# Performance work log

Measured on AMD Instinct MI355X. Metric: run time of the kernel, lower is better.

Reference implementation:

```python
import jax, jax.numpy as jnp
import numpy as np

L, D, H, DR, KF = 2, 256, 8, 64, 4   # n_layer, d_model, n_head, d_rpe, k_feedforward
B, S, T = 2, 256, 256
LN_EPS = 1e-5


def _ln(x, g, b):
    m = jnp.mean(x, -1, keepdims=True)
    v = jnp.mean((x - m) ** 2, -1, keepdims=True)
    return (x - m) * jax.lax.rsqrt(v + LN_EPS) * g + b


def _attn_rpe(q_in, kv_in, rpe, tgt_mask, wq, bq, wk, bk, wv, bv, wo, bo, wr, br):
    # RPE-biased multi-head cross attention: rpe -> (rpe_k, rpe_v) added per (src,tgt) pair.
    Bq, Sq, _ = q_in.shape
    Tk = kv_in.shape[1]
    Dh = D // H
    q = (q_in @ wq + bq).reshape(Bq, Sq, H, Dh)
    k = (kv_in @ wk + bk).reshape(Bq, Tk, H, Dh)
    v = (kv_in @ wv + bv).reshape(Bq, Tk, H, Dh)
    r = rpe @ wr + br                                   # [B,S,T,2D]
    rk, rv = jnp.split(r, 2, axis=-1)
    rk = rk.reshape(Bq, Sq, Tk, H, Dh)
    rv = rv.reshape(Bq, Sq, Tk, H, Dh)
    scale = 1.0 / np.sqrt(Dh).astype(np.float32)
    scores = (jnp.einsum('bshd,bthd->bhst', q, k)
              + jnp.einsum('bshd,bsthd->bhst', q, rk)) * scale
    scores = jnp.where(tgt_mask[:, None, None, :], -jnp.inf, scores)
    w = jax.nn.softmax(scores, axis=-1)                 # [B,H,S,T]
    out = (jnp.einsum('bhst,bthd->bshd', w, v)
           + jnp.einsum('bhst,bsthd->bshd', w, rv))
    return out.reshape(Bq, Sq, D) @ wo + bo


def _forward(src, tgt, rpe, src_padding_mask, tgt_padding_mask, p):
    for i in range(L):  # loop over n_layer (structurally distinct params)
        s2 = _ln(src, p['ln1_g'][i], p['ln1_b'][i])
        tn = _ln(tgt, p['lnt_g'][i], p['lnt_b'][i])
        a = _attn_rpe(s2, tn, rpe, tgt_padding_mask,
                      p['wq'][i], p['bq'][i], p['wk'][i], p['bk'][i],
                      p['wv'][i], p['bv'][i], p['wo'][i], p['bo'][i],
                      p['wr'][i], p['br'][i])
        src = src + a
        s2 = _ln(src, p['ln2_g'][i], p['ln2_b'][i])
        s2 = jax.nn.relu(s2 @ p['w1'][i] + p['b1'][i]) @ p['w2'][i] + p['b2'][i]
        src = src + s2
        src = jnp.where(src_padding_mask[:, :, None], 0.0, src)
    return src


def setup_inputs() -> dict:
    key = jax.random.key(0)
    ks = jax.random.split(key, 16)
    f = lambda k, shp: (0.02 * jax.random.normal(k, shp)).astype(jnp.float32)
    return {
        'src': jax.random.normal(ks[0], (B, S, D), jnp.float32),
        'tgt': jax.random.normal(ks[1], (B, T, D), jnp.float32),
        'rpe': jax.random.normal(ks[2], (B, S, T, DR), jnp.float32),
        'src_padding_mask': jax.random.bernoulli(ks[3], 0.05, (B, S)),
        'tgt_padding_mask': jax.random.bernoulli(ks[4], 0.1, (B, T)),
        'ln1_g': jnp.ones((L, D), jnp.float32), 'ln1_b': jnp.zeros((L, D), jnp.float32),
        'lnt_g': jnp.ones((L, D), jnp.float32), 'lnt_b': jnp.zeros((L, D), jnp.float32),
        'ln2_g': jnp.ones((L, D), jnp.float32), 'ln2_b': jnp.zeros((L, D), jnp.float32),
        'wq': f(ks[5], (L, D, D)), 'bq': jnp.zeros((L, D), jnp.float32),
        'wk': f(ks[6], (L, D, D)), 'bk': jnp.zeros((L, D), jnp.float32),
        'wv': f(ks[7], (L, D, D)), 'bv': jnp.zeros((L, D), jnp.float32),
        'wo': f(ks[8], (L, D, D)), 'bo': jnp.zeros((L, D), jnp.float32),
        'wr': f(ks[9], (L, DR, 2 * D)), 'br': jnp.zeros((L, 2 * D), jnp.float32),
        'w1': f(ks[10], (L, D, KF * D)), 'b1': jnp.zeros((L, KF * D), jnp.float32),
        'w2': f(ks[11], (L, KF * D, D)), 'b2': jnp.zeros((L, D), jnp.float32),
    }


def reference(src, tgt, rpe, src_padding_mask, tgt_padding_mask,
              ln1_g, ln1_b, lnt_g, lnt_b, ln2_g, ln2_b,
              wq, bq, wk, bk, wv, bv, wo, bo, wr, br, w1, b1, w2, b2):
    p = dict(ln1_g=ln1_g, ln1_b=ln1_b, lnt_g=lnt_g, lnt_b=lnt_b,
             ln2_g=ln2_g, ln2_b=ln2_b, wq=wq, bq=bq, wk=wk, bk=bk,
             wv=wv, bv=bv, wo=wo, bo=bo, wr=wr, br=br,
             w1=w1, b1=b1, w2=w2, b2=b2)
    return _forward(src, tgt, rpe, src_padding_mask, tgt_padding_mask, p)
```

## Files before the change

kernel.cpp:

```cpp
#include <hip/hip_runtime.h>
#include <math.h>

#define ROWS 512
#define DMODEL 256
#define NH 8
#define DH 32
#define NEG_INF -1e30f

__global__ __launch_bounds__(64) void ln_qt_kernel(
    const float* __restrict__ src, const float* __restrict__ tgt,
    const float* __restrict__ g1, const float* __restrict__ b1,
    const float* __restrict__ gt, const float* __restrict__ bt,
    const float* __restrict__ bo,
    float* __restrict__ S2, float* __restrict__ TNb, float* __restrict__ X)
{
  int row = blockIdx.x;
  const float* x; float* o; const float* g; const float* b;
  if (row < ROWS) { x = src + row * DMODEL; o = S2 + row * DMODEL; g = g1; b = b1; }
  else { int r = row - ROWS; x = tgt + r * DMODEL; o = TNb + r * DMODEL; g = gt; b = bt; }
  int lane = threadIdx.x;
  float4 v = ((const float4*)x)[lane];
  float s  = v.x + v.y + v.z + v.w;
  float ss = v.x*v.x + v.y*v.y + v.z*v.z + v.w*v.w;
#pragma unroll
  for (int off = 32; off >= 1; off >>= 1) {
    s  += __shfl_xor(s,  off);
    ss += __shfl_xor(ss, off);
  }
  float mean = s * (1.0f / 256.0f);
  float var  = ss * (1.0f / 256.0f) - mean * mean;
  float rstd = rsqrtf(var + 1e-5f);
  float4 gg = ((const float4*)g)[lane];
  float4 bb = ((const float4*)b)[lane];
  float4 ov;
  ov.x = (v.x - mean) * rstd * gg.x + bb.x;
  ov.y = (v.y - mean) * rstd * gg.y + bb.y;
  ov.z = (v.z - mean) * rstd * gg.z + bb.z;
  ov.w = (v.w - mean) * rstd * gg.w + bb.w;
  ((float4*)o)[lane] = ov;
  if (row < ROWS) {
    float4 bov = ((const float4*)bo)[lane];
    float4 xi;
    xi.x = v.x + bov.x; xi.y = v.y + bov.y; xi.z = v.z + bov.z; xi.w = v.w + bov.w;
    ((float4*)(X + row * DMODEL))[lane] = xi;
  }
}

__global__ __launch_bounds__(64) void ln2_kernel(
    const float* __restrict__ X, const float* __restrict__ g, const float* __restrict__ b,
    const float* __restrict__ b2, const int* __restrict__ smask,
    float* __restrict__ XN, float* __restrict__ outinit)
{
  int row = blockIdx.x;
  int lane = threadIdx.x;
  float4 v = ((const float4*)(X + row * DMODEL))[lane];
  float s  = v.x + v.y + v.z + v.w;
  float ss = v.x*v.x + v.y*v.y + v.z*v.z + v.w*v.w;
#pragma unroll
  for (int off = 32; off >= 1; off >>= 1) {
    s  += __shfl_xor(s,  off);
    ss += __shfl_xor(ss, off);
  }
  float mean = s * (1.0f / 256.0f);
  float var  = ss * (1.0f / 256.0f) - mean * mean;
  float rstd = rsqrtf(var + 1e-5f);
  float4 gg = ((const float4*)g)[lane];
  float4 bb = ((const float4*)b)[lane];
  float4 ov;
  ov.x = (v.x - mean) * rstd * gg.x + bb.x;
  ov.y = (v.y - mean) * rstd * gg.y + bb.y;
  ov.z = (v.z - mean) * rstd * gg.z + bb.z;
  ov.w = (v.w - mean) * rstd * gg.w + bb.w;
  ((float4*)(XN + row * DMODEL))[lane] = ov;
  float mm = (smask[row] != 0) ? 0.0f : 1.0f;
  float4 b2v = ((const float4*)b2)[lane];
  float4 oi;
  oi.x = mm * (v.x + b2v.x);
  oi.y = mm * (v.y + b2v.y);
  oi.z = mm * (v.z + b2v.z);
  oi.w = mm * (v.w + b2v.w);
  ((float4*)(outinit + row * DMODEL))[lane] = oi;
}

__device__ __forceinline__ void gemm_core32(
    const float* __restrict__ A, int lda,
    const float* __restrict__ Bw, int ldb,
    int kbeg, int kend, int m0, int n0,
    float acc[2][4])
{
  __shared__ float At[32][34];
  __shared__ float Bs[32][64];
  int tid = threadIdx.x;
  int tx = tid & 15, ty = tid >> 4;
  int r  = tid >> 3;
  int c4 = tid & 7;
  for (int kc = kbeg; kc < kend; kc += 32) {
    float4 a = *(const float4*)(A + (size_t)(m0 + r) * lda + kc + c4 * 4);
    const float* bp = Bw + (size_t)(kc + r) * ldb + n0;
    float4 b0 = *(const float4*)(bp + c4 * 4);
    float4 b1v = *(const float4*)(bp + 32 + c4 * 4);
    At[c4*4+0][r] = a.x; At[c4*4+1][r] = a.y; At[c4*4+2][r] = a.z; At[c4*4+3][r] = a.w;
    *(float4*)&Bs[r][c4*4]      = b0;
    *(float4*)&Bs[r][32 + c4*4] = b1v;
    __syncthreads();
#pragma unroll
    for (int k = 0; k < 32; ++k) {
      float2 av = *(const float2*)&At[k][ty * 2];
      float4 bv = *(const float4*)&Bs[k][tx * 4];
      acc[0][0] = fmaf(av.x, bv.x, acc[0][0]); acc[0][1] = fmaf(av.x, bv.y, acc[0][1]);
      acc[0][2] = fmaf(av.x, bv.z, acc[0][2]); acc[0][3] = fmaf(av.x, bv.w, acc[0][3]);
      acc[1][0] = fmaf(av.y, bv.x, acc[1][0]); acc[1][1] = fmaf(av.y, bv.y, acc[1][1]);
      acc[1][2] = fmaf(av.y, bv.z, acc[1][2]); acc[1][3] = fmaf(av.y, bv.w, acc[1][3]);
    }
    __syncthreads();
  }
}

__global__ __launch_bounds__(256) void qkv_kernel(
    const float* __restrict__ S2, const float* __restrict__ TNb,
    const float* __restrict__ wq, const float* __restrict__ wk, const float* __restrict__ wv,
    const float* __restrict__ bq, const float* __restrict__ bk, const float* __restrict__ bv,
    float* __restrict__ Qb, float* __restrict__ Kb, float* __restrict__ Vb)
{
  int z = blockIdx.z;
  const float* A    = (z == 0) ? S2 : TNb;
  const float* Bw   = (z == 0) ? wq : (z == 1) ? wk : wv;
  const float* bias = (z == 0) ? bq : (z == 1) ? bk : bv;
  int m0 = blockIdx.y * 32, n0 = blockIdx.x * 64;
  float acc[2][4] = {};
  gemm_core32(A, DMODEL, Bw, DMODEL, 0, DMODEL, m0, n0, acc);
  int tid = threadIdx.x, tx = tid & 15, ty = tid >> 4;
  int c0 = n0 + tx * 4;
  const float scale = 0.1767766952966369f;
#pragma unroll
  for (int i = 0; i < 2; ++i) {
    int m = m0 + ty * 2 + i;
    float4 r;
    r.x = acc[i][0] + bias[c0 + 0];
    r.y = acc[i][1] + bias[c0 + 1];
    r.z = acc[i][2] + bias[c0 + 2];
    r.w = acc[i][3] + bias[c0 + 3];
    if (z == 0) {
      r.x *= scale; r.y *= scale; r.z *= scale; r.w *= scale;
      *(float4*)&Qb[m * DMODEL + c0] = r;
    } else {
      int b = m >> 8, t = m & 255, h = c0 >> 5, d0 = c0 & 31;
      float* dst = ((z == 1) ? Kb : Vb) + (size_t)(b * NH + h) * 8192 + t * DH + d0;
      *(float4*)dst = r;
    }
  }
}

__global__ __launch_bounds__(256) void wo_kernel(
    const float* __restrict__ AO, const float* __restrict__ wo,
    float* __restrict__ X)
{
  int m0 = blockIdx.y * 32, n0 = blockIdx.x * 64;
  int kbeg = blockIdx.z * 128;
  float acc[2][4] = {};
  gemm_core32(AO, DMODEL, wo, DMODEL, kbeg, kbeg + 128, m0, n0, acc);
  int tid = threadIdx.x, tx = tid & 15, ty = tid >> 4;
  int c0 = n0 + tx * 4;
#pragma unroll
  for (int i = 0; i < 2; ++i) {
    int m = m0 + ty * 2 + i;
    atomicAdd(&X[m * DMODEL + c0 + 0], acc[i][0]);
    atomicAdd(&X[m * DMODEL + c0 + 1], acc[i][1]);
    atomicAdd(&X[m * DMODEL + c0 + 2], acc[i][2]);
    atomicAdd(&X[m * DMODEL + c0 + 3], acc[i][3]);
  }
}

__global__ __launch_bounds__(256) void ff1_kernel(
    const float* __restrict__ XN, const float* __restrict__ w1, const float* __restrict__ b1,
    float* __restrict__ H1)
{
  int m0 = blockIdx.y * 32, n0 = blockIdx.x * 64;
  float acc[2][4] = {};
  gemm_core32(XN, DMODEL, w1, 1024, 0, DMODEL, m0, n0, acc);
  int tid = threadIdx.x, tx = tid & 15, ty = tid >> 4;
  int c0 = n0 + tx * 4;
#pragma unroll
  for (int i = 0; i < 2; ++i) {
    int m = m0 + ty * 2 + i;
    float4 r;
    r.x = fmaxf(acc[i][0] + b1[c0 + 0], 0.0f);
    r.y = fmaxf(acc[i][1] + b1[c0 + 1], 0.0f);
    r.z = fmaxf(acc[i][2] + b1[c0 + 2], 0.0f);
    r.w = fmaxf(acc[i][3] + b1[c0 + 3], 0.0f);
    *(float4*)&H1[m * 1024 + c0] = r;
  }
}

__global__ __launch_bounds__(256) void ff2_kernel(
    const float* __restrict__ H1, const float* __restrict__ w2,
    const int* __restrict__ smask, float* __restrict__ outb)
{
  int m0 = blockIdx.y * 32, n0 = blockIdx.x * 64;
  int kbeg = blockIdx.z * 256;
  float acc[2][4] = {};
  gemm_core32(H1, 1024, w2, DMODEL, kbeg, kbeg + 256, m0, n0, acc);
  int tid = threadIdx.x, tx = tid & 15, ty = tid >> 4;
  int c0 = n0 + tx * 4;
#pragma unroll
  for (int i = 0; i < 2; ++i) {
    int m = m0 + ty * 2 + i;
    float mm = (smask[m] != 0) ? 0.0f : 1.0f;
    atomicAdd(&outb[m * DMODEL + c0 + 0], mm * acc[i][0]);
    atomicAdd(&outb[m * DMODEL + c0 + 1], mm * acc[i][1]);
    atomicAdd(&outb[m * DMODEL + c0 + 2], mm * acc[i][2]);
    atomicAdd(&outb[m * DMODEL + c0 + 3], mm * acc[i][3]);
  }
}

__global__ __launch_bounds__(256) void attn_kernel(
    const float* __restrict__ Qb, const float* __restrict__ Kb, const float* __restrict__ Vb,
    const float* __restrict__ rpe, const int* __restrict__ tmask,
    const float* __restrict__ wrl, const float* __restrict__ brl,
    float* __restrict__ AO)
{
  __shared__ float Ks[256][32];
  __shared__ float Vt[32][260];
  __shared__ float ps[4][256];
  __shared__ float qs[16][32];
  __shared__ float wks[5][32];
  __shared__ float wvs[5][32];
  int bid = blockIdx.x;
  int b = bid >> 7, h = (bid >> 4) & 7, s0 = (bid & 15) << 4;
  int tid = threadIdx.x;
  const float* Kp = Kb + (size_t)(b * NH + h) * 8192;
  const float* Vp = Vb + (size_t)(b * NH + h) * 8192;
  {
    int t = tid;
    const float4* kr = (const float4*)(Kp + t * DH);
    const float4* vr = (const float4*)(Vp + t * DH);
    int sw = t & 7;
#pragma unroll
    for (int c = 0; c < 8; ++c) {
      float4 k4 = kr[c];
      *(float4*)&Ks[t][(c ^ sw) * 4] = k4;
    }
#pragma unroll
    for (int c = 0; c < 8; ++c) {
      float4 v4 = vr[c];
      Vt[c*4+0][t] = v4.x; Vt[c*4+1][t] = v4.y; Vt[c*4+2][t] = v4.z; Vt[c*4+3][t] = v4.w;
    }
  }
  if (tid < 160) {
    int j = tid >> 5, d = tid & 31;
    wks[j][d] = (j < 4) ? wrl[j * 512 + h * DH + d]       : brl[h * DH + d];
    wvs[j][d] = (j < 4) ? wrl[j * 512 + 256 + h * DH + d] : brl[256 + h * DH + d];
  }
  if (tid >= 128) {
    int u = tid - 128;
    int rr = u >> 3, cc = u & 7;
    *(float4*)&qs[rr][cc*4] =
        *(const float4*)&Qb[(b * 256 + s0 + rr) * DMODEL + h * DH + cc * 4];
  }
  __syncthreads();

  int w = tid >> 6, lane = tid & 63;
  int msk[4];
#pragma unroll
  for (int it = 0; it < 4; ++it) msk[it] = tmask[b * 256 + it * 64 + lane];

  for (int i = 0; i < 4; ++i) {
    int sl = w * 4 + i;
    int s = s0 + sl;
    float4 q4[8];
#pragma unroll
    for (int c = 0; c < 8; ++c) q4[c] = *(const float4*)&qs[sl][c * 4];
    float qw[4]; float qbr = 0.0f;
#pragma unroll
    for (int j = 0; j < 4; ++j) {
      float t0 = 0;
#pragma unroll
      for (int c = 0; c < 8; ++c) {
        float4 wv4 = *(const float4*)&wks[j][c * 4];
        t0 += q4[c].x*wv4.x + q4[c].y*wv4.y + q4[c].z*wv4.z + q4[c].w*wv4.w;
      }
      qw[j] = t0;
    }
#pragma unroll
    for (int c = 0; c < 8; ++c) {
      float4 wv4 = *(const float4*)&wks[4][c * 4];
      qbr += q4[c].x*wv4.x + q4[c].y*wv4.y + q4[c].z*wv4.z + q4[c].w*wv4.w;
    }
    const float4* rp4 = (const float4*)(rpe + (size_t)(b * 256 + s) * 1024);
    float sc[4]; float4 rr[4];
#pragma unroll
    for (int it = 0; it < 4; ++it) {
      int t = it * 64 + lane;
      int sw = t & 7;
      float sv = 0;
#pragma unroll
      for (int c = 0; c < 8; ++c) {
        float4 k4 = *(const float4*)&Ks[t][(c ^ sw) * 4];
        sv = fmaf(q4[c].x, k4.x, sv); sv = fmaf(q4[c].y, k4.y, sv);
        sv = fmaf(q4[c].z, k4.z, sv); sv = fmaf(q4[c].w, k4.w, sv);
      }
      float4 rv = rp4[t];
      rr[it] = rv;
      sv += rv.x*qw[0] + rv.y*qw[1] + rv.z*qw[2] + rv.w*qw[3] + qbr;
      if (msk[it] != 0) sv = NEG_INF;
      sc[it] = sv;
    }
    float mval = fmaxf(fmaxf(sc[0], sc[1]), fmaxf(sc[2], sc[3]));
#pragma unroll
    for (int off = 32; off >= 1; off >>= 1) mval = fmaxf(mval, __shfl_xor(mval, off));
    float p[4], lsum = 0;
#pragma unroll
    for (int it = 0; it < 4; ++it) { p[it] = __expf(sc[it] - mval); lsum += p[it]; }
    float wj0 = 0, wj1 = 0, wj2 = 0, wj3 = 0;
#pragma unroll
    for (int it = 0; it < 4; ++it) {
      wj0 = fmaf(p[it], rr[it].x, wj0);
      wj1 = fmaf(p[it], rr[it].y, wj1);
      wj2 = fmaf(p[it], rr[it].z, wj2);
      wj3 = fmaf(p[it], rr[it].w, wj3);
    }
#pragma unroll
    for (int off = 32; off >= 1; off >>= 1) {
      lsum += __shfl_xor(lsum, off);
      wj0 += __shfl_xor(wj0, off);
      wj1 += __shfl_xor(wj1, off);
      wj2 += __shfl_xor(wj2, off);
      wj3 += __shfl_xor(wj3, off);
    }
#pragma unroll
    for (int it = 0; it < 4; ++it) ps[w][it * 64 + lane] = p[it];
    int g = lane >> 5, d = lane & 31;
    float o = 0;
#pragma unroll
    for (int n = 0; n < 32; ++n) {
      int t = g * 128 + n * 4;
      float4 p4 = *(const float4*)&ps[w][t];
      float4 v4 = *(const float4*)&Vt[d][t];
      o += p4.x*v4.x + p4.y*v4.y + p4.z*v4.z + p4.w*v4.w;
    }
    o += __shfl_xor(o, 32);
    float corr = wj0 * wvs[0][d] + wj1 * wvs[1][d] + wj2 * wvs[2][d] + wj3 * wvs[3][d];
    float oval = (o + corr) / lsum + wvs[4][d];
    if (lane < 32) AO[(b * 256 + s) * DMODEL + h * DH + d] = oval;
  }
}

extern "C" void kernel_launch(void* const* d_in, const int* in_sizes, int n_in,
                              void* d_out, int out_size, void* d_ws, size_t ws_size,
                              hipStream_t stream)
{
  const float* src  = (const float*)d_in[0];
  const float* tgt  = (const float*)d_in[1];
  const float* rpe  = (const float*)d_in[2];
  const int*   smask = (const int*)d_in[3];
  const int*   tmask = (const int*)d_in[4];
  const float* ln1g = (const float*)d_in[5];
  const float* ln1b = (const float*)d_in[6];
  const float* lntg = (const float*)d_in[7];
  const float* lntb = (const float*)d_in[8];
  const float* ln2g = (const float*)d_in[9];
  const float* ln2b = (const float*)d_in[10];
  const float* wq = (const float*)d_in[11];
  const float* bq = (const float*)d_in[12];
  const float* wk = (const float*)d_in[13];
  const float* bk = (const float*)d_in[14];
  const float* wv = (const float*)d_in[15];
  const float* bv = (const float*)d_in[16];
  const float* wo = (const float*)d_in[17];
  const float* bo = (const float*)d_in[18];
  const float* wr = (const float*)d_in[19];
  const float* br = (const float*)d_in[20];
  const float* w1 = (const float*)d_in[21];
  const float* b1 = (const float*)d_in[22];
  const float* w2 = (const float*)d_in[23];
  const float* b2 = (const float*)d_in[24];

  float* w    = (float*)d_ws;
  float* S2   = w;
  float* TNb  = w + 131072;
  float* Qb   = w + 262144;
  float* Kb   = w + 393216;
  float* Vb   = w + 524288;
  float* AO   = w + 655360;
  float* X    = w + 786432;
  float* XN   = w + 917504;
  float* SRC1 = w + 1048576;
  float* H1   = w + 1179648;

  for (int l = 0; l < 2; ++l) {
    const float* srcin = l ? SRC1 : src;
    float* outb = l ? (float*)d_out : SRC1;
    ln_qt_kernel<<<1024, 64, 0, stream>>>(srcin, tgt, ln1g + l*256, ln1b + l*256,
                                          lntg + l*256, lntb + l*256, bo + l*256,
                                          S2, TNb, X);
    qkv_kernel<<<dim3(4, 16, 3), 256, 0, stream>>>(S2, TNb,
                                                   wq + l*65536, wk + l*65536, wv + l*65536,
                                                   bq + l*256, bk + l*256, bv + l*256,
                                                   Qb, Kb, Vb);
    attn_kernel<<<256, 256, 0, stream>>>(Qb, Kb, Vb, rpe, tmask,
                                         wr + l*2048, br + l*512, AO);
    wo_kernel<<<dim3(4, 16, 2), 256, 0, stream>>>(AO, wo + l*65536, X);
    ln2_kernel<<<512, 64, 0, stream>>>(X, ln2g + l*256, ln2b + l*256, b2 + l*256,
                                       smask, XN, outb);
    ff1_kernel<<<dim3(16, 16), 256, 0, stream>>>(XN, w1 + l*262144, b1 + l*1024, H1);
    ff2_kernel<<<dim3(4, 16, 4), 256, 0, stream>>>(H1, w2 + l*262144, smask, outb);
  }
}
```

Before: 262.8 us.

## Fuse all layer stages into one persistent kernel with grid barriers

Replaces the fourteen per-stage kernel launches with a single persistent 256-block kernel. Stages are separated by software grid-wide barriers built on an atomic counter, and shared memory is a union of the attention and GEMM layouts. The aim is to remove launch overhead and inter-kernel gaps. In exchange it relies on all 256 blocks being co-resident to avoid deadlock, adds barrier spin cost, and changes the split-K factor of the wo GEMM.

```diff
diff --git a/kernel.cpp b/kernel.cpp
--- a/kernel.cpp
+++ b/kernel.cpp
@@ -1,103 +1,53 @@
 #include <hip/hip_runtime.h>
 #include <math.h>
 
-#define ROWS 512
-#define DMODEL 256
-#define NH 8
-#define DH 32
 #define NEG_INF -1e30f
 
-__global__ __launch_bounds__(64) void ln_qt_kernel(
-    const float* __restrict__ src, const float* __restrict__ tgt,
-    const float* __restrict__ g1, const float* __restrict__ b1,
-    const float* __restrict__ gt, const float* __restrict__ bt,
-    const float* __restrict__ bo,
-    float* __restrict__ S2, float* __restrict__ TNb, float* __restrict__ X)
-{
-  int row = blockIdx.x;
-  const float* x; float* o; const float* g; const float* b;
-  if (row < ROWS) { x = src + row * DMODEL; o = S2 + row * DMODEL; g = g1; b = b1; }
-  else { int r = row - ROWS; x = tgt + r * DMODEL; o = TNb + r * DMODEL; g = gt; b = bt; }
-  int lane = threadIdx.x;
-  float4 v = ((const float4*)x)[lane];
-  float s  = v.x + v.y + v.z + v.w;
-  float ss = v.x*v.x + v.y*v.y + v.z*v.z + v.w*v.w;
-#pragma unroll
-  for (int off = 32; off >= 1; off >>= 1) {
-    s  += __shfl_xor(s,  off);
-    ss += __shfl_xor(ss, off);
+struct AttnLds {
+  float Ks[256][32];
+  float Vt[32][260];
+  float ps[4][256];
+  float qs[16][32];
+  float wks[5][32];
+  float wvs[5][32];
+};
+struct GemmLds {
+  float At[32][34];
+  float Bs[32][64];
+};
+union MegaLds {
+  AttnLds a;
+  GemmLds g;
+  float pad[20608];
+};
+
+__device__ __forceinline__ void gbar(unsigned* cnt, unsigned expect) {
+  __syncthreads();
+  if (threadIdx.x == 0) {
+    __threadfence();
+    __hip_atomic_fetch_add(cnt, 1u, __ATOMIC_RELEASE, __HIP_MEMORY_SCOPE_AGENT);
+    while (__hip_atomic_load(cnt, __ATOMIC_RELAXED, __HIP_MEMORY_SCOPE_AGENT) < expect)
+      __builtin_amdgcn_s_sleep(2);
+    __threadfence();
   }
-  float mean = s * (1.0f / 256.0f);
-  float var  = ss * (1.0f / 256.0f) - mean * mean;
-  float rstd = rsqrtf(var + 1e-5f);
-  float4 gg = ((const float4*)g)[lane];
-  float4 bb = ((const float4*)b)[lane];
-  float4 ov;
-  ov.x = (v.x - mean) * rstd * gg.x + bb.x;
-  ov.y = (v.y - mean) * rstd * gg.y + bb.y;
-  ov.z = (v.z - mean) * rstd * gg.z + bb.z;
-  ov.w = (v.w - mean) * rstd * gg.w + bb.w;
-  ((float4*)o)[lane] = ov;
-  if (row < ROWS) {
-    float4 bov = ((const float4*)bo)[lane];
-    float4 xi;
-    xi.x = v.x + bov.x; xi.y = v.y + bov.y; xi.z = v.z + bov.z; xi.w = v.w + bov.w;
-    ((float4*)(X + row * DMODEL))[lane] = xi;
-  }
+  __syncthreads();
 }
 
-__global__ __launch_bounds__(64) void ln2_kernel(
-    const float* __restrict__ X, const float* __restrict__ g, const float* __restrict__ b,
-    const float* __restrict__ b2, const int* __restrict__ smask,
-    float* __restrict__ XN, float* __restrict__ outinit)
-{
-  int row = blockIdx.x;
-  int lane = threadIdx.x;
-  float4 v = ((const float4*)(X + row * DMODEL))[lane];
-  float s  = v.x + v.y + v.z + v.w;
-  float ss = v.x*v.x + v.y*v.y + v.z*v.z + v.w*v.w;
-#pragma unroll
-  for (int off = 32; off >= 1; off >>= 1) {
-    s  += __shfl_xor(s,  off);
-    ss += __shfl_xor(ss, off);
-  }
-  float mean = s * (1.0f / 256.0f);
-  float var  = ss * (1.0f / 256.0f) - mean * mean;
-  float rstd = rsqrtf(var + 1e-5f);
-  float4 gg = ((const float4*)g)[lane];
-  float4 bb = ((const float4*)b)[lane];
-  float4 ov;
-  ov.x = (v.x - mean) * rstd * gg.x + bb.x;
-  ov.y = (v.y - mean) * rstd * gg.y + bb.y;
-  ov.z = (v.z - mean) * rstd * gg.z + bb.z;
-  ov.w = (v.w - mean) * rstd * gg.w + bb.w;
-  ((float4*)(XN + row * DMODEL))[lane] = ov;
-  float mm = (smask[row] != 0) ? 0.0f : 1.0f;
-  float4 b2v = ((const float4*)b2)[lane];
-  float4 oi;
-  oi.x = mm * (v.x + b2v.x);
-  oi.y = mm * (v.y + b2v.y);
-  oi.z = mm * (v.z + b2v.z);
-  oi.w = mm * (v.w + b2v.w);
-  ((float4*)(outinit + row * DMODEL))[lane] = oi;
-}
-
-__device__ __forceinline__ void gemm_core32(
+__device__ __forceinline__ void gemm32(MegaLds& L,
     const float* __restrict__ A, int lda,
     const float* __restrict__ Bw, int ldb,
-    int kbeg, int kend, int m0, int n0,
-    float acc[2][4])
+    int kbeg, int kend, int m0, int n0, float acc[2][4])
 {
-  __shared__ float At[32][34];
-  __shared__ float Bs[32][64];
+  float (&At)[32][34] = L.g.At;
+  float (&Bs)[32][64] = L.g.Bs;
   int tid = threadIdx.x;
-  int tx = tid & 15, ty = tid >> 4;
   int r  = tid >> 3;
   int c4 = tid & 7;
+  int tx = tid & 15, ty = tid >> 4;
   for (int kc = kbeg; kc < kend; kc += 32) {
     float4 a = *(const float4*)(A + (size_t)(m0 + r) * lda + kc + c4 * 4);
     const float* bp = Bw + (size_t)(kc + r) * ldb + n0;
-    float4 b0 = *(const float4*)(bp + c4 * 4);
+    float4 b0  = *(const float4*)(bp + c4 * 4);
     float4 b1v = *(const float4*)(bp + 32 + c4 * 4);
     At[c4*4+0][r] = a.x; At[c4*4+1][r] = a.y; At[c4*4+2][r] = a.z; At[c4*4+3][r] = a.w;
     *(float4*)&Bs[r][c4*4]      = b0;
@@ -116,232 +66,327 @@
   }
 }
 
-__global__ __launch_bounds__(256) void qkv_kernel(
-    const float* __restrict__ S2, const float* __restrict__ TNb,
-    const float* __restrict__ wq, const float* __restrict__ wk, const float* __restrict__ wv,
-    const float* __restrict__ bq, const float* __restrict__ bk, const float* __restrict__ bv,
-    float* __restrict__ Qb, float* __restrict__ Kb, float* __restrict__ Vb)
+__global__ __launch_bounds__(256, 1) void mega_kernel(
+    const float* __restrict__ src, const float* __restrict__ tgt,
+    const float* __restrict__ rpe,
+    const int* __restrict__ smask, const int* __restrict__ tmask,
+    const float* __restrict__ ln1g, const float* __restrict__ ln1b,
+    const float* __restrict__ lntg, const float* __restrict__ lntb,
+    const float* __restrict__ ln2g, const float* __restrict__ ln2b,
+    const float* __restrict__ wq, const float* __restrict__ bq,
+    const float* __restrict__ wk, const float* __restrict__ bk,
+    const float* __restrict__ wv, const float* __restrict__ bv,
+    const float* __restrict__ wo, const float* __restrict__ bo,
+    const float* __restrict__ wr, const float* __restrict__ br,
+    const float* __restrict__ w1, const float* __restrict__ b1,
+    const float* __restrict__ w2, const float* __restrict__ b2,
+    float* __restrict__ ws, float* __restrict__ out, unsigned* __restrict__ cnt)
 {
-  int z = blockIdx.z;
-  const float* A    = (z == 0) ? S2 : TNb;
-  const float* Bw   = (z == 0) ? wq : (z == 1) ? wk : wv;
-  const float* bias = (z == 0) ? bq : (z == 1) ? bk : bv;
-  int m0 = blockIdx.y * 32, n0 = blockIdx.x * 64;
-  float acc[2][4] = {};
-  gemm_core32(A, DMODEL, Bw, DMODEL, 0, DMODEL, m0, n0, acc);
-  int tid = threadIdx.x, tx = tid & 15, ty = tid >> 4;
-  int c0 = n0 + tx * 4;
-  const float scale = 0.1767766952966369f;
-#pragma unroll
-  for (int i = 0; i < 2; ++i) {
-    int m = m0 + ty * 2 + i;
-    float4 r;
-    r.x = acc[i][0] + bias[c0 + 0];
-    r.y = acc[i][1] + bias[c0 + 1];
-    r.z = acc[i][2] + bias[c0 + 2];
-    r.w = acc[i][3] + bias[c0 + 3];
-    if (z == 0) {
-      r.x *= scale; r.y *= scale; r.z *= scale; r.w *= scale;
-      *(float4*)&Qb[m * DMODEL + c0] = r;
-    } else {
-      int b = m >> 8, t = m & 255, h = c0 >> 5, d0 = c0 & 31;
-      float* dst = ((z == 1) ? Kb : Vb) + (size_t)(b * NH + h) * 8192 + t * DH + d0;
-      *(float4*)dst = r;
-    }
-  }
-}
-
-__global__ __launch_bounds__(256) void wo_kernel(
-    const float* __restrict__ AO, const float* __restrict__ wo,
-    float* __restrict__ X)
-{
-  int m0 = blockIdx.y * 32, n0 = blockIdx.x * 64;
-  int kbeg = blockIdx.z * 128;
-  float acc[2][4] = {};
-  gemm_core32(AO, DMODEL, wo, DMODEL, kbeg, kbeg + 128, m0, n0, acc);
-  int tid = threadIdx.x, tx = tid & 15, ty = tid >> 4;
-  int c0 = n0 + tx * 4;
-#pragma unroll
-  for (int i = 0; i < 2; ++i) {
-    int m = m0 + ty * 2 + i;
-    atomicAdd(&X[m * DMODEL + c0 + 0], acc[i][0]);
-    atomicAdd(&X[m * DMODEL + c0 + 1], acc[i][1]);
-    atomicAdd(&X[m * DMODEL + c0 + 2], acc[i][2]);
-    atomicAdd(&X[m * DMODEL + c0 + 3], acc[i][3]);
-  }
-}
-
-__global__ __launch_bounds__(256) void ff1_kernel(
-    const float* __restrict__ XN, const float* __restrict__ w1, const float* __restrict__ b1,
-    float* __restrict__ H1)
-{
-  int m0 = blockIdx.y * 32, n0 = blockIdx.x * 64;
-  float acc[2][4] = {};
-  gemm_core32(XN, DMODEL, w1, 1024, 0, DMODEL, m0, n0, acc);
-  int tid = threadIdx.x, tx = tid & 15, ty = tid >> 4;
-  int c0 = n0 + tx * 4;
-#pragma unroll
-  for (int i = 0; i < 2; ++i) {
-    int m = m0 + ty * 2 + i;
-    float4 r;
-    r.x = fmaxf(acc[i][0] + b1[c0 + 0], 0.0f);
-    r.y = fmaxf(acc[i][1] + b1[c0 + 1], 0.0f);
-    r.z = fmaxf(acc[i][2] + b1[c0 + 2], 0.0f);
-    r.w = fmaxf(acc[i][3] + b1[c0 + 3], 0.0f);
-    *(float4*)&H1[m * 1024 + c0] = r;
-  }
-}
-
-__global__ __launch_bounds__(256) void ff2_kernel(
-    const float* __restrict__ H1, const float* __restrict__ w2,
-    const int* __restrict__ smask, float* __restrict__ outb)
-{
-  int m0 = blockIdx.y * 32, n0 = blockIdx.x * 64;
-  int kbeg = blockIdx.z * 256;
-  float acc[2][4] = {};
-  gemm_core32(H1, 1024, w2, DMODEL, kbeg, kbeg + 256, m0, n0, acc);
-  int tid = threadIdx.x, tx = tid & 15, ty = tid >> 4;
-  int c0 = n0 + tx * 4;
-#pragma unroll
-  for (int i = 0; i < 2; ++i) {
-    int m = m0 + ty * 2 + i;
-    float mm = (smask[m] != 0) ? 0.0f : 1.0f;
-    atomicAdd(&outb[m * DMODEL + c0 + 0], mm * acc[i][0]);
-    atomicAdd(&outb[m * DMODEL + c0 + 1], mm * acc[i][1]);
-    atomicAdd(&outb[m * DMODEL + c0 + 2], mm * acc[i][2]);
-    atomicAdd(&outb[m * DMODEL + c0 + 3], mm * acc[i][3]);
-  }
-}
-
-__global__ __launch_bounds__(256) void attn_kernel(
-    const float* __restrict__ Qb, const float* __restrict__ Kb, const float* __restrict__ Vb,
-    const float* __restrict__ rpe, const int* __restrict__ tmask,
-    const float* __restrict__ wrl, const float* __restrict__ brl,
-    float* __restrict__ AO)
-{
-  __shared__ float Ks[256][32];
-  __shared__ float Vt[32][260];
-  __shared__ float ps[4][256];
-  __shared__ float qs[16][32];
-  __shared__ float wks[5][32];
-  __shared__ float wvs[5][32];
-  int bid = blockIdx.x;
-  int b = bid >> 7, h = (bid >> 4) & 7, s0 = (bid & 15) << 4;
-  int tid = threadIdx.x;
-  const float* Kp = Kb + (size_t)(b * NH + h) * 8192;
-  const float* Vp = Vb + (size_t)(b * NH + h) * 8192;
-  {
-    int t = tid;
-    const float4* kr = (const float4*)(Kp + t * DH);
-    const float4* vr = (const float4*)(Vp + t * DH);
-    int sw = t & 7;
-#pragma unroll
-    for (int c = 0; c < 8; ++c) {
-      float4 k4 = kr[c];
-      *(float4*)&Ks[t][(c ^ sw) * 4] = k4;
-    }
-#pragma unroll
-    for (int c = 0; c < 8; ++c) {
-      float4 v4 = vr[c];
-      Vt[c*4+0][t] = v4.x; Vt[c*4+1][t] = v4.y; Vt[c*4+2][t] = v4.z; Vt[c*4+3][t] = v4.w;
-    }
-  }
-  if (tid < 160) {
-    int j = tid >> 5, d = tid & 31;
-    wks[j][d] = (j < 4) ? wrl[j * 512 + h * DH + d]       : brl[h * DH + d];
-    wvs[j][d] = (j < 4) ? wrl[j * 512 + 256 + h * DH + d] : brl[256 + h * DH + d];
-  }
-  if (tid >= 128) {
-    int u = tid - 128;
-    int rr = u >> 3, cc = u & 7;
-    *(float4*)&qs[rr][cc*4] =
-        *(const float4*)&Qb[(b * 256 + s0 + rr) * DMODEL + h * DH + cc * 4];
-  }
-  __syncthreads();
-
+  __shared__ MegaLds L;
+  int tid = threadIdx.x, bx = blockIdx.x;
   int w = tid >> 6, lane = tid & 63;
-  int msk[4];
-#pragma unroll
-  for (int it = 0; it < 4; ++it) msk[it] = tmask[b * 256 + it * 64 + lane];
-
-  for (int i = 0; i < 4; ++i) {
-    int sl = w * 4 + i;
-    int s = s0 + sl;
-    float4 q4[8];
-#pragma unroll
-    for (int c = 0; c < 8; ++c) q4[c] = *(const float4*)&qs[sl][c * 4];
-    float qw[4]; float qbr = 0.0f;
-#pragma unroll
-    for (int j = 0; j < 4; ++j) {
-      float t0 = 0;
-#pragma unroll
-      for (int c = 0; c < 8; ++c) {
-        float4 wv4 = *(const float4*)&wks[j][c * 4];
-        t0 += q4[c].x*wv4.x + q4[c].y*wv4.y + q4[c].z*wv4.z + q4[c].w*wv4.w;
-      }
-      qw[j] = t0;
-    }
-#pragma unroll
-    for (int c = 0; c < 8; ++c) {
-      float4 wv4 = *(const float4*)&wks[4][c * 4];
-      qbr += q4[c].x*wv4.x + q4[c].y*wv4.y + q4[c].z*wv4.z + q4[c].w*wv4.w;
-    }
-    const float4* rp4 = (const float4*)(rpe + (size_t)(b * 256 + s) * 1024);
-    float sc[4]; float4 rr[4];
-#pragma unroll
-    for (int it = 0; it < 4; ++it) {
-      int t = it * 64 + lane;
-      int sw = t & 7;
-      float sv = 0;
-#pragma unroll
-      for (int c = 0; c < 8; ++c) {
-        float4 k4 = *(const float4*)&Ks[t][(c ^ sw) * 4];
-        sv = fmaf(q4[c].x, k4.x, sv); sv = fmaf(q4[c].y, k4.y, sv);
-        sv = fmaf(q4[c].z, k4.z, sv); sv = fmaf(q4[c].w, k4.w, sv);
-      }
-      float4 rv = rp4[t];
-      rr[it] = rv;
-      sv += rv.x*qw[0] + rv.y*qw[1] + rv.z*qw[2] + rv.w*qw[3] + qbr;
-      if (msk[it] != 0) sv = NEG_INF;
-      sc[it] = sv;
-    }
-    float mval = fmaxf(fmaxf(sc[0], sc[1]), fmaxf(sc[2], sc[3]));
-#pragma unroll
-    for (int off = 32; off >= 1; off >>= 1) mval = fmaxf(mval, __shfl_xor(mval, off));
-    float p[4], lsum = 0;
-#pragma unroll
-    for (int it = 0; it < 4; ++it) { p[it] = __expf(sc[it] - mval); lsum += p[it]; }
-    float wj0 = 0, wj1 = 0, wj2 = 0, wj3 = 0;
-#pragma unroll
-    for (int it = 0; it < 4; ++it) {
-      wj0 = fmaf(p[it], rr[it].x, wj0);
-      wj1 = fmaf(p[it], rr[it].y, wj1);
-      wj2 = fmaf(p[it], rr[it].z, wj2);
-      wj3 = fmaf(p[it], rr[it].w, wj3);
-    }
-#pragma unroll
-    for (int off = 32; off >= 1; off >>= 1) {
-      lsum += __shfl_xor(lsum, off);
-      wj0 += __shfl_xor(wj0, off);
-      wj1 += __shfl_xor(wj1, off);
-      wj2 += __shfl_xor(wj2, off);
-      wj3 += __shfl_xor(wj3, off);
-    }
-#pragma unroll
-    for (int it = 0; it < 4; ++it) ps[w][it * 64 + lane] = p[it];
-    int g = lane >> 5, d = lane & 31;
-    float o = 0;
-#pragma unroll
-    for (int n = 0; n < 32; ++n) {
-      int t = g * 128 + n * 4;
-      float4 p4 = *(const float4*)&ps[w][t];
-      float4 v4 = *(const float4*)&Vt[d][t];
-      o += p4.x*v4.x + p4.y*v4.y + p4.z*v4.z + p4.w*v4.w;
-    }
-    o += __shfl_xor(o, 32);
-    float corr = wj0 * wvs[0][d] + wj1 * wvs[1][d] + wj2 * wvs[2][d] + wj3 * wvs[3][d];
-    float oval = (o + corr) / lsum + wvs[4][d];
-    if (lane < 32) AO[(b * 256 + s) * DMODEL + h * DH + d] = oval;
+  unsigned bi = 0;
+
+  float* S2   = ws;
+  float* TN   = ws + 131072;
+  float* Qb   = ws + 262144;
+  float* Kb   = ws + 393216;
+  float* Vb   = ws + 524288;
+  float* AO   = ws + 655360;
+  float* X    = ws + 786432;
+  float* XN   = ws + 917504;
+  float* SRC1 = ws + 1048576;
+  float* H1   = ws + 1179648;
+
+  for (int l = 0; l < 2; ++l) {
+    const float* srcin = l ? SRC1 : src;
+    float* outb = l ? out : SRC1;
+    const float* g1 = ln1g + l*256; const float* be1 = ln1b + l*256;
+    const float* gt = lntg + l*256; const float* bet = lntb + l*256;
+    const float* g2 = ln2g + l*256; const float* be2 = ln2b + l*256;
+    const float* wq_l = wq + l*65536; const float* bq_l = bq + l*256;
+    const float* wk_l = wk + l*65536; const float* bk_l = bk + l*256;
+    const float* wv_l = wv + l*65536; const float* bv_l = bv + l*256;
+    const float* wo_l = wo + l*65536; const float* bo_l = bo + l*256;
+    const float* wr_l = wr + l*2048;  const float* br_l = br + l*512;
+    const float* w1_l = w1 + l*262144; const float* b1_l = b1 + l*1024;
+    const float* w2_l = w2 + l*262144; const float* b2_l = b2 + l*256;
+
+    {
+      int task = bx * 4 + w;
+      bool issrc = task < 512;
+      int r = issrc ? task : task - 512;
+      const float* xrow = issrc ? srcin + r * 256 : tgt + r * 256;
+      float* orow       = issrc ? S2 + r * 256    : TN + r * 256;
+      const float* g    = issrc ? g1 : gt;
+      const float* bb   = issrc ? be1 : bet;
+      float4 v = ((const float4*)xrow)[lane];
+      float s  = v.x + v.y + v.z + v.w;
+      float ss = v.x*v.x + v.y*v.y + v.z*v.z + v.w*v.w;
+#pragma unroll
+      for (int off = 32; off >= 1; off >>= 1) {
+        s  += __shfl_xor(s,  off);
+        ss += __shfl_xor(ss, off);
+      }
+      float mean = s * (1.0f / 256.0f);
+      float var  = ss * (1.0f / 256.0f) - mean * mean;
+      float rstd = rsqrtf(var + 1e-5f);
+      float4 gg = ((const float4*)g)[lane];
+      float4 b4 = ((const float4*)bb)[lane];
+      float4 ov;
+      ov.x = (v.x - mean) * rstd * gg.x + b4.x;
+      ov.y = (v.y - mean) * rstd * gg.y + b4.y;
+      ov.z = (v.z - mean) * rstd * gg.z + b4.z;
+      ov.w = (v.w - mean) * rstd * gg.w + b4.w;
+      ((float4*)orow)[lane] = ov;
+      if (issrc) {
+        float4 bov = ((const float4*)bo_l)[lane];
+        float4 xi;
+        xi.x = v.x + bov.x; xi.y = v.y + bov.y; xi.z = v.z + bov.z; xi.w = v.w + bov.w;
+        ((float4*)(X + r * 256))[lane] = xi;
+      }
+    }
+    gbar(cnt, ++bi * 256u);
+
+    if (bx < 192) {
+      int z = bx >> 6, u = bx & 63;
+      int m0 = (u >> 2) * 32, n0 = (u & 3) * 64;
+      const float* A    = (z == 0) ? S2 : TN;
+      const float* Bw   = (z == 0) ? wq_l : (z == 1) ? wk_l : wv_l;
+      const float* bias = (z == 0) ? bq_l : (z == 1) ? bk_l : bv_l;
+      float acc[2][4] = {};
+      gemm32(L, A, 256, Bw, 256, 0, 256, m0, n0, acc);
+      int tx = tid & 15, ty = tid >> 4;
+      int c0 = n0 + tx * 4;
+      const float scale = 0.1767766952966369f;
+#pragma unroll
+      for (int i = 0; i < 2; ++i) {
+        int m = m0 + ty * 2 + i;
+        float4 r;
+        r.x = acc[i][0] + bias[c0 + 0];
+        r.y = acc[i][1] + bias[c0 + 1];
+        r.z = acc[i][2] + bias[c0 + 2];
+        r.w = acc[i][3] + bias[c0 + 3];
+        if (z == 0) {
+          r.x *= scale; r.y *= scale; r.z *= scale; r.w *= scale;
+          *(float4*)&Qb[m * 256 + c0] = r;
+        } else {
+          int b = m >> 8, t = m & 255, h = c0 >> 5, d0 = c0 & 31;
+          float* dst = ((z == 1) ? Kb : Vb) + (size_t)(b * 8 + h) * 8192 + t * 32 + d0;
+          *(float4*)dst = r;
+        }
+      }
+    }
+    gbar(cnt, ++bi * 256u);
+
+    {
+      int b = bx >> 7, h = (bx >> 4) & 7, s0 = (bx & 15) << 4;
+      const float* Kp = Kb + (size_t)(b * 8 + h) * 8192;
+      const float* Vp = Vb + (size_t)(b * 8 + h) * 8192;
+      {
+        int t = tid;
+        const float4* kr = (const float4*)(Kp + t * 32);
+        const float4* vr = (const float4*)(Vp + t * 32);
+        int sw = t & 7;
+#pragma unroll
+        for (int c = 0; c < 8; ++c) {
+          float4 k4 = kr[c];
+          *(float4*)&L.a.Ks[t][(c ^ sw) * 4] = k4;
+        }
+#pragma unroll
+        for (int c = 0; c < 8; ++c) {
+          float4 v4 = vr[c];
+          L.a.Vt[c*4+0][t] = v4.x; L.a.Vt[c*4+1][t] = v4.y;
+          L.a.Vt[c*4+2][t] = v4.z; L.a.Vt[c*4+3][t] = v4.w;
+        }
+      }
+      if (tid < 160) {
+        int j = tid >> 5, d = tid & 31;
+        L.a.wks[j][d] = (j < 4) ? wr_l[j * 512 + h * 32 + d]       : br_l[h * 32 + d];
+        L.a.wvs[j][d] = (j < 4) ? wr_l[j * 512 + 256 + h * 32 + d] : br_l[256 + h * 32 + d];
+      }
+      if (tid >= 128) {
+        int u = tid - 128;
+        int rr2 = u >> 3, cc = u & 7;
+        *(float4*)&L.a.qs[rr2][cc*4] =
+            *(const float4*)&Qb[(b * 256 + s0 + rr2) * 256 + h * 32 + cc * 4];
+      }
+      __syncthreads();
+
+      int msk[4];
+#pragma unroll
+      for (int it = 0; it < 4; ++it) msk[it] = tmask[b * 256 + it * 64 + lane];
+
+      for (int i = 0; i < 4; ++i) {
+        int sl = w * 4 + i;
+        int s = s0 + sl;
+        float4 q4[8];
+#pragma unroll
+        for (int c = 0; c < 8; ++c) q4[c] = *(const float4*)&L.a.qs[sl][c * 4];
+        float qw[4]; float qbr = 0.0f;
+#pragma unroll
+        for (int j = 0; j < 4; ++j) {
+          float t0 = 0;
+#pragma unroll
+          for (int c = 0; c < 8; ++c) {
+            float4 wv4 = *(const float4*)&L.a.wks[j][c * 4];
+            t0 += q4[c].x*wv4.x + q4[c].y*wv4.y + q4[c].z*wv4.z + q4[c].w*wv4.w;
+          }
+          qw[j] = t0;
+        }
+#pragma unroll
+        for (int c = 0; c < 8; ++c) {
+          float4 wv4 = *(const float4*)&L.a.wks[4][c * 4];
+          qbr += q4[c].x*wv4.x + q4[c].y*wv4.y + q4[c].z*wv4.z + q4[c].w*wv4.w;
+        }
+        const float4* rp4 = (const float4*)(rpe + (size_t)(b * 256 + s) * 1024);
+        float sc[4]; float4 rr[4];
+#pragma unroll
+        for (int it = 0; it < 4; ++it) {
+          int t = it * 64 + lane;
+          int sw = t & 7;
+          float sv = 0;
+#pragma unroll
+          for (int c = 0; c < 8; ++c) {
+            float4 k4 = *(const float4*)&L.a.Ks[t][(c ^ sw) * 4];
+            sv = fmaf(q4[c].x, k4.x, sv); sv = fmaf(q4[c].y, k4.y, sv);
+            sv = fmaf(q4[c].z, k4.z, sv); sv = fmaf(q4[c].w, k4.w, sv);
+          }
+          float4 rv = rp4[t];
+          rr[it] = rv;
+          sv += rv.x*qw[0] + rv.y*qw[1] + rv.z*qw[2] + rv.w*qw[3] + qbr;
+          if (msk[it] != 0) sv = NEG_INF;
+          sc[it] = sv;
+        }
+        float mval = fmaxf(fmaxf(sc[0], sc[1]), fmaxf(sc[2], sc[3]));
+#pragma unroll
+        for (int off = 32; off >= 1; off >>= 1) mval = fmaxf(mval, __shfl_xor(mval, off));
+        float p[4], lsum = 0;
+#pragma unroll
+        for (int it = 0; it < 4; ++it) { p[it] = __expf(sc[it] - mval); lsum += p[it]; }
+        float wj0 = 0, wj1 = 0, wj2 = 0, wj3 = 0;
+#pragma unroll
+        for (int it = 0; it < 4; ++it) {
+          wj0 = fmaf(p[it], rr[it].x, wj0);
+          wj1 = fmaf(p[it], rr[it].y, wj1);
+          wj2 = fmaf(p[it], rr[it].z, wj2);
+          wj3 = fmaf(p[it], rr[it].w, wj3);
+        }
+#pragma unroll
+        for (int off = 32; off >= 1; off >>= 1) {
+          lsum += __shfl_xor(lsum, off);
+          wj0 += __shfl_xor(wj0, off);
+          wj1 += __shfl_xor(wj1, off);
+          wj2 += __shfl_xor(wj2, off);
+          wj3 += __shfl_xor(wj3, off);
+        }
+#pragma unroll
+        for (int it = 0; it < 4; ++it) L.a.ps[w][it * 64 + lane] = p[it];
+        int g = lane >> 5, d = lane & 31;
+        float o = 0;
+#pragma unroll
+        for (int n = 0; n < 32; ++n) {
+          int t = g * 128 + n * 4;
+          float4 p4 = *(const float4*)&L.a.ps[w][t];
+          float4 v4 = *(const float4*)&L.a.Vt[d][t];
+          o += p4.x*v4.x + p4.y*v4.y + p4.z*v4.z + p4.w*v4.w;
+        }
+        o += __shfl_xor(o, 32);
+        float corr = wj0 * L.a.wvs[0][d] + wj1 * L.a.wvs[1][d]
+                   + wj2 * L.a.wvs[2][d] + wj3 * L.a.wvs[3][d];
+        float oval = (o + corr) / lsum + L.a.wvs[4][d];
+        if (lane < 32) AO[(b * 256 + s) * 256 + h * 32 + d] = oval;
+      }
+    }
+    gbar(cnt, ++bi * 256u);
+
+    {
+      int ks = bx >> 6, u = bx & 63;
+      int m0 = (u >> 2) * 32, n0 = (u & 3) * 64;
+      float acc[2][4] = {};
+      gemm32(L, AO, 256, wo_l, 256, ks * 64, ks * 64 + 64, m0, n0, acc);
+      int tx = tid & 15, ty = tid >> 4;
+      int c0 = n0 + tx * 4;
+#pragma unroll
+      for (int i = 0; i < 2; ++i) {
+        int m = m0 + ty * 2 + i;
+        atomicAdd(&X[m * 256 + c0 + 0], acc[i][0]);
+        atomicAdd(&X[m * 256 + c0 + 1], acc[i][1]);
+        atomicAdd(&X[m * 256 + c0 + 2], acc[i][2]);
+        atomicAdd(&X[m * 256 + c0 + 3], acc[i][3]);
+      }
+    }
+    gbar(cnt, ++bi * 256u);
+
+    if (w < 2) {
+      int row = bx * 2 + w;
+      float4 v = ((const float4*)(X + row * 256))[lane];
+      float s  = v.x + v.y + v.z + v.w;
+      float ss = v.x*v.x + v.y*v.y + v.z*v.z + v.w*v.w;
+#pragma unroll
+      for (int off = 32; off >= 1; off >>= 1) {
+        s  += __shfl_xor(s,  off);
+        ss += __shfl_xor(ss, off);
+      }
+      float mean = s * (1.0f / 256.0f);
+      float var  = ss * (1.0f / 256.0f) - mean * mean;
+      float rstd = rsqrtf(var + 1e-5f);
+      float4 gg = ((const float4*)g2)[lane];
+      float4 b4 = ((const float4*)be2)[lane];
+      float4 ov;
+      ov.x = (v.x - mean) * rstd * gg.x + b4.x;
+      ov.y = (v.y - mean) * rstd * gg.y + b4.y;
+      ov.z = (v.z - mean) * rstd * gg.z + b4.z;
+      ov.w = (v.w - mean) * rstd * gg.w + b4.w;
+      ((float4*)(XN + row * 256))[lane] = ov;
+      float mm = (smask[row] != 0) ? 0.0f : 1.0f;
+      float4 b2v = ((const float4*)b2_l)[lane];
+      float4 oi;
+      oi.x = mm * (v.x + b2v.x);
+      oi.y = mm * (v.y + b2v.y);
+      oi.z = mm * (v.z + b2v.z);
+      oi.w = mm * (v.w + b2v.w);
+      ((float4*)(outb + row * 256))[lane] = oi;
+    }
+    gbar(cnt, ++bi * 256u);
+
+    {
+      int m0 = (bx >> 4) * 32, n0 = (bx & 15) * 64;
+      float acc[2][4] = {};
+      gemm32(L, XN, 256, w1_l, 1024, 0, 256, m0, n0, acc);
+      int tx = tid & 15, ty = tid >> 4;
+      int c0 = n0 + tx * 4;
+#pragma unroll
+      for (int i = 0; i < 2; ++i) {
+        int m = m0 + ty * 2 + i;
+        float4 r;
+        r.x = fmaxf(acc[i][0] + b1_l[c0 + 0], 0.0f);
+        r.y = fmaxf(acc[i][1] + b1_l[c0 + 1], 0.0f);
+        r.z = fmaxf(acc[i][2] + b1_l[c0 + 2], 0.0f);
+        r.w = fmaxf(acc[i][3] + b1_l[c0 + 3], 0.0f);
+        *(float4*)&H1[m * 1024 + c0] = r;
+      }
+    }
+    gbar(cnt, ++bi * 256u);
+
+    {
+      int ks = bx >> 6, u = bx & 63;
+      int m0 = (u >> 2) * 32, n0 = (u & 3) * 64;
+      float acc[2][4] = {};
+      gemm32(L, H1, 1024, w2_l, 256, ks * 256, ks * 256 + 256, m0, n0, acc);
+      int tx = tid & 15, ty = tid >> 4;
+      int c0 = n0 + tx * 4;
+#pragma unroll
+      for (int i = 0; i < 2; ++i) {
+        int m = m0 + ty * 2 + i;
+        float mm = (smask[m] != 0) ? 0.0f : 1.0f;
+        atomicAdd(&outb[m * 256 + c0 + 0], mm * acc[i][0]);
+        atomicAdd(&outb[m * 256 + c0 + 1], mm * acc[i][1]);
+        atomicAdd(&outb[m * 256 + c0 + 2], mm * acc[i][2]);
+        atomicAdd(&outb[m * 256 + c0 + 3], mm * acc[i][3]);
+      }
+    }
+    if (l == 0) gbar(cnt, ++bi * 256u);
   }
 }
 
@@ -375,34 +420,13 @@
   const float* w2 = (const float*)d_in[23];
   const float* b2 = (const float*)d_in[24];
 
-  float* w    = (float*)d_ws;
-  float* S2   = w;
-  float* TNb  = w + 131072;
-  float* Qb   = w + 262144;
-  float* Kb   = w + 393216;
-  float* Vb   = w + 524288;
-  float* AO   = w + 655360;
-  float* X    = w + 786432;
-  float* XN   = w + 917504;
-  float* SRC1 = w + 1048576;
-  float* H1   = w + 1179648;
-
-  for (int l = 0; l < 2; ++l) {
-    const float* srcin = l ? SRC1 : src;
-    float* outb = l ? (float*)d_out : SRC1;
-    ln_qt_kernel<<<1024, 64, 0, stream>>>(srcin, tgt, ln1g + l*256, ln1b + l*256,
-                                          lntg + l*256, lntb + l*256, bo + l*256,
-                                          S2, TNb, X);
-    qkv_kernel<<<dim3(4, 16, 3), 256, 0, stream>>>(S2, TNb,
-                                                   wq + l*65536, wk + l*65536, wv + l*65536,
-                                                   bq + l*256, bk + l*256, bv + l*256,
-                                                   Qb, Kb, Vb);
-    attn_kernel<<<256, 256, 0, stream>>>(Qb, Kb, Vb, rpe, tmask,
-                                         wr + l*2048, br + l*512, AO);
-    wo_kernel<<<dim3(4, 16, 2), 256, 0, stream>>>(AO, wo + l*65536, X);
-    ln2_kernel<<<512, 64, 0, stream>>>(X, ln2g + l*256, ln2b + l*256, b2 + l*256,
-                                       smask, XN, outb);
-    ff1_kernel<<<dim3(16, 16), 256, 0, stream>>>(XN, w1 + l*262144, b1 + l*1024, H1);
-    ff2_kernel<<<dim3(4, 16, 4), 256, 0, stream>>>(H1, w2 + l*262144, smask, outb);
-  }
+  float* ws = (float*)d_ws;
+  unsigned* cnt = (unsigned*)(ws + 1703936);
+
+  hipMemsetAsync(cnt, 0, 64, stream);
+  mega_kernel<<<256, 256, 0, stream>>>(
+      src, tgt, rpe, smask, tmask,
+      ln1g, ln1b, lntg, lntb, ln2g, ln2b,
+      wq, bq, wk, bk, wv, bv, wo, bo, wr, br, w1, b1, w2, b2,
+      ws, (float*)d_out, cnt);
 }
```

Measured after the change: 541.9 us. 2.06x slower.
